# Kernel tuning notes

Measured on AMD Instinct MI355X. Metric: run time of the kernel, lower is better.

Reference implementation:

```python
import math
import jax, jax.numpy as jnp
import numpy as np

B, S, DM = 2, 1024, 1024
H, D = 16, 64
BUCKETS, MAX_POS = 256, 512
SPAN = BUCKETS          # pos_ebd_size = position_buckets
SCALE = math.sqrt(D * 3)  # scale_factor = 1 + len([c2p, p2c])
EPS = 1e-7


def _make_log_bucket_position(rel, bucket_size, max_position):
    # numpy, matches make_log_bucket_position exactly (static, shape-derived)
    sign = np.sign(rel)
    mid = bucket_size // 2
    abs_pos = np.where((rel < mid) & (rel > -mid), mid - 1, np.abs(rel))
    log_pos = np.ceil(np.log(abs_pos / mid) / np.log((max_position - 1) / mid) * (mid - 1)) + mid
    return np.where(abs_pos <= mid, rel, (log_pos * sign)).astype(np.int64)


def _build_relative_position(q_size, k_size):
    rel = np.arange(q_size)[:, None] - np.arange(k_size)[None, :]
    return _make_log_bucket_position(rel, BUCKETS, MAX_POS)  # [q, k]


def setup_inputs() -> dict:
    key = jax.random.key(0)
    ks = jax.random.split(key, 12)
    w = lambda k, sh: (jax.random.normal(k, sh, jnp.float32) * 0.02)
    return {
        "hidden_states": jax.random.normal(ks[0], (B, S, DM), jnp.float32),
        "rel_embeddings": jax.random.normal(ks[1], (2 * SPAN, DM), jnp.float32),
        "Wq": w(ks[2], (DM, DM)), "bq": jnp.zeros((DM,), jnp.float32),
        "Wk": w(ks[3], (DM, DM)), "bk": jnp.zeros((DM,), jnp.float32),
        "Wv": w(ks[4], (DM, DM)), "bv": jnp.zeros((DM,), jnp.float32),
        "Wo": w(ks[5], (DM, DM)), "bo": jnp.zeros((DM,), jnp.float32),
        "ln_w": jnp.ones((DM,), jnp.float32), "ln_b": jnp.zeros((DM,), jnp.float32),
        "attention_mask": jnp.ones((B, 1, S, S), jnp.int32),
    }


def reference(hidden_states, rel_embeddings, Wq, bq, Wk, bk, Wv, bv, Wo, bo, ln_w, ln_b, attention_mask):
    b, s, _ = hidden_states.shape
    heads = lambda x: x.reshape(b, s, H, D).transpose(0, 2, 1, 3)  # [B,H,S,D]
    q = heads(hidden_states @ Wq + bq)
    k = heads(hidden_states @ Wk + bk)
    v = heads(hidden_states @ Wv + bv)

    # content-to-content scores
    scores = jnp.einsum('bhqd,bhkd->bhqk', q, k) / SCALE

    # disentangled relative-position bias (share_att_key=True: reuse key/query proj)
    rel = _build_relative_position(s, s)                      # [S,S] static int
    c2p_idx = np.clip(rel + SPAN, 0, 2 * SPAN - 1)            # [S,S]
    p2c_idx = np.clip(-rel + SPAN, 0, 2 * SPAN - 1)           # [S,S]
    pos_k = (rel_embeddings @ Wk + bk).reshape(2 * SPAN, H, D).transpose(1, 0, 2)  # [H,P,D]
    pos_q = (rel_embeddings @ Wq + bq).reshape(2 * SPAN, H, D).transpose(1, 0, 2)  # [H,P,D]

    qi = np.arange(s)[:, None]  # row index for gather along bucket axis
    c2p = jnp.einsum('bhqd,hpd->bhqp', q, pos_k)              # [B,H,S,2K]
    scores = scores + c2p[:, :, qi, c2p_idx] / SCALE          # gather -> [B,H,S,S]
    p2c = jnp.einsum('bhkd,hpd->bhkp', k, pos_q)              # [B,H,S,2K]
    scores = scores + jnp.swapaxes(p2c[:, :, qi, p2c_idx], -1, -2) / SCALE

    # XSoftmax: masked softmax, masked positions zeroed
    m = attention_mask.astype(bool)
    probs = jax.nn.softmax(jnp.where(m, scores, -jnp.inf), axis=-1)
    probs = jnp.where(m, probs, 0.0)

    ctx = jnp.einsum('bhqk,bhkd->bhqd', probs, v).transpose(0, 2, 1, 3).reshape(b, s, H * D)

    # DebertaV2SelfOutput: dense + (eval-mode dropout = identity) + LayerNorm residual
    h = ctx @ Wo + bo + hidden_states
    mu = h.mean(-1, keepdims=True)
    var = ((h - mu) ** 2).mean(-1, keepdims=True)
    return (h - mu) * jax.lax.rsqrt(var + EPS) * ln_w + ln_b
```

## Files before the change

### kernel.cpp

```cpp
#include <hip/hip_runtime.h>
#include <hip/hip_bf16.h>

#define Sv   1024
#define DMv  1024
#define Hv   16
#define PBv  512
#define INVSCALE 0.07216878364870322f

typedef unsigned short u16;
typedef unsigned int   u32;
typedef short  short8  __attribute__((ext_vector_type(8)));
typedef float  float4v __attribute__((ext_vector_type(4)));

__device__ __forceinline__ float b2f(u16 u) {
    union { u32 u; float f; } c; c.u = ((u32)u) << 16; return c.f;
}
__device__ __forceinline__ u16 f2b(float f) {
    union { float f; u32 u; } c; c.f = f;
    u32 u = c.u;
    return (u16)((u + 0x7fffu + ((u >> 16) & 1u)) >> 16);
}
__device__ __forceinline__ float ldE(const void* p, size_t i, bool f32) {
    return f32 ? ((const float*)p)[i] : b2f(((const u16*)p)[i]);
}

__device__ __forceinline__ void gld16(const u16* g, u16* l) {
    __builtin_amdgcn_global_load_lds(
        (const __attribute__((address_space(1))) void*)g,
        (__attribute__((address_space(3))) void*)l,
        16, 0, 0);
}

__global__ void setup_kernel(const u32* __restrict__ w, int* __restrict__ flag,
                             int* __restrict__ tbl) {
    if (blockIdx.x == 0) {
        int t = threadIdx.x;
        if (t < 64) {
            int c = 0;
            #pragma unroll
            for (int i = 0; i < 4; i++) {
                u32 v = w[t * 4 + i];
                c += (((v >> 23) & 0xFFu) < 0x80u) ? 1 : 0;
            }
            #pragma unroll
            for (int off = 32; off > 0; off >>= 1) c += __shfl_down(c, off, 64);
            if (t == 0) *flag = (c > 128) ? 1 : 0;
        }
        return;
    }
    int i = (blockIdx.x - 1) * 256 + threadIdx.x;
    if (i >= 2047) return;
    int rel = i - 1023;
    const int mid = 128;
    int abs_pos = (rel < mid && rel > -mid) ? (mid - 1) : (rel < 0 ? -rel : rel);
    int bucket;
    if (abs_pos <= mid) {
        bucket = rel;
    } else {
        double lp = ceil(log((double)abs_pos / 128.0) / log(511.0 / 128.0) * 127.0) + 128.0;
        bucket = (int)lp * (rel > 0 ? 1 : -1);
    }
    int idx = bucket + 256;
    idx = idx < 0 ? 0 : (idx > 511 ? 511 : idx);
    tbl[i] = idx;
}

__global__ __launch_bounds__(256) void cvt2_kernel(
    const void* __restrict__ s0, u16* __restrict__ d0,
    const void* __restrict__ s1, u16* __restrict__ d1,
    const int* __restrict__ flagp)
{
    bool f32 = (*flagp != 0);
    const void* src; u16* dst; size_t i;
    if (blockIdx.x < 1024) {
        src = s0; dst = d0;
        i = ((size_t)blockIdx.x * 256 + threadIdx.x) * 8;
    } else {
        src = s1; dst = d1;
        i = ((size_t)(blockIdx.x - 1024) * 256 + threadIdx.x) * 8;
    }
    if (f32) {
        const float* s = (const float*)src + i;
        float4 a = *(const float4*)s;
        float4 b = *(const float4*)(s + 4);
        uint4 o = make_uint4(f2b(a.x) | (f2b(a.y) << 16), f2b(a.z) | (f2b(a.w) << 16),
                             f2b(b.x) | (f2b(b.y) << 16), f2b(b.z) | (f2b(b.w) << 16));
        *(uint4*)(dst + i) = o;
    } else {
        *(uint4*)(dst + i) = *(const uint4*)((const u16*)src + i);
    }
}

__global__ __launch_bounds__(256) void transpose_cvt(
    const void* __restrict__ S0, const void* __restrict__ S1,
    const void* __restrict__ S2, const void* __restrict__ S3,
    u16* __restrict__ out, u16* __restrict__ out3,
    const int* __restrict__ flagp)
{
    bool f32 = (*flagp != 0);
    int z = blockIdx.z;
    const void* S = (z == 0) ? S0 : (z == 1) ? S1 : (z == 2) ? S2 : S3;
    u16* O = (z < 3) ? (out + (size_t)z * 1048576) : out3;
    int k0 = blockIdx.x * 64, n0 = blockIdx.y * 64;
    __shared__ u16 Ls[64][72];
    int t = threadIdx.x;
    int r = t >> 2, cseg = (t & 3) * 16;

    u16 v[16];
    size_t base = (size_t)(k0 + r) * 1024 + n0 + cseg;
    if (f32) {
        const float* p = (const float*)S + base;
        #pragma unroll
        for (int i = 0; i < 16; i += 4) {
            float4 f = *(const float4*)(p + i);
            v[i] = f2b(f.x); v[i + 1] = f2b(f.y); v[i + 2] = f2b(f.z); v[i + 3] = f2b(f.w);
        }
    } else {
        const u16* p = (const u16*)S + base;
        uint4 a = *(const uint4*)p, b = *(const uint4*)(p + 8);
        u32 wd[8] = {a.x, a.y, a.z, a.w, b.x, b.y, b.z, b.w};
        #pragma unroll
        for (int i = 0; i < 8; i++) { v[2 * i] = (u16)(wd[i] & 0xffff); v[2 * i + 1] = (u16)(wd[i] >> 16); }
    }
    #pragma unroll
    for (int i = 0; i < 16; i++) Ls[cseg + i][r] = v[i];
    __syncthreads();

    int n = t >> 2, kseg = (t & 3) * 16;
    u16* op = O + (size_t)(n0 + n) * 1024 + k0 + kseg;
    *(uint4*)op       = *(const uint4*)&Ls[n][kseg];
    *(uint4*)(op + 8) = *(const uint4*)&Ls[n][kseg + 8];
}

__global__ __launch_bounds__(256) void wgemm_bt(
    const u16* __restrict__ A,
    const u16* __restrict__ B0, const u16* __restrict__ B1, const u16* __restrict__ B2,
    const void* __restrict__ b0, const void* __restrict__ b1, const void* __restrict__ b2,
    u16* __restrict__ O0, u16* __restrict__ O1, u16* __restrict__ O2,
    const int* __restrict__ flagp, int vseg, int sseg)
{
    bool f32 = (*flagp != 0);
    __shared__ u16 As[128][64];
    __shared__ u16 Bs[128][64];

    int t = threadIdx.x;
    int seg = blockIdx.x >> 3;
    int n0  = (blockIdx.x & 7) * 128;
    int m0  = blockIdx.y * 128;
    const u16* Bt = (seg == 0) ? B0 : (seg == 1) ? B1 : B2;
    const void* bi = (seg == 0) ? b0 : (seg == 1) ? b1 : b2;
    u16* O = (seg == 0) ? O0 : (seg == 1) ? O1 : O2;
    float es = (seg == sseg) ? INVSCALE : 1.0f;

    int w = t >> 6, lane = t & 63;
    int quad = lane >> 4, l16 = lane & 15;
    int wm = (w >> 1) * 64, wn = (w & 1) * 64;

    float4v acc[4][4];
    #pragma unroll
    for (int i = 0; i < 4; i++)
        #pragma unroll
        for (int j = 0; j < 4; j++)
            acc[i][j] = (float4v){0.f, 0.f, 0.f, 0.f};

    int lr8  = lane >> 3;
    int lcol = (lane & 7) * 8;
    const u16* ap0 = A  + (size_t)(m0 + w * 32 + lr8) * 1024 + lcol;
    const u16* bp0 = Bt + (size_t)(n0 + w * 32 + lr8) * 1024 + lcol;

    for (int k0 = 0; k0 < 1024; k0 += 64) {
        __syncthreads();
        #pragma unroll
        for (int i = 0; i < 4; i++) {
            gld16(ap0 + (size_t)(i * 8) * 1024 + k0, &As[w * 32 + i * 8][0]);
            gld16(bp0 + (size_t)(i * 8) * 1024 + k0, &Bs[w * 32 + i * 8][0]);
        }
        __syncthreads();

        #pragma unroll
        for (int kk = 0; kk < 64; kk += 32) {
            short8 af[4], bf[4];
            #pragma unroll
            for (int i = 0; i < 4; i++)
                af[i] = *(const short8*)&As[wm + i * 16 + l16][kk + quad * 8];
            #pragma unroll
            for (int j = 0; j < 4; j++)
                bf[j] = *(const short8*)&Bs[wn + j * 16 + l16][kk + quad * 8];
            #pragma unroll
            for (int j = 0; j < 4; j++)
                #pragma unroll
                for (int i = 0; i < 4; i++)
                    acc[i][j] = __builtin_amdgcn_mfma_f32_16x16x32_bf16(af[i], bf[j], acc[i][j], 0, 0, 0);
        }
    }

    if (seg == vseg) {
        #pragma unroll
        for (int j = 0; j < 4; j++) {
            int ncol = n0 + wn + j * 16 + l16;
            float bv = ldE(bi, ncol, f32);
            u16* obase = O + (size_t)(ncol >> 6) * 131072 + (size_t)(ncol & 63) * 2048;
            #pragma unroll
            for (int i = 0; i < 4; i++) {
                int rbase = m0 + wm + i * 16 + quad * 4;
                u32 w0 = (u32)f2b((acc[i][j][0] + bv) * es) | ((u32)f2b((acc[i][j][1] + bv) * es) << 16);
                u32 w1 = (u32)f2b((acc[i][j][2] + bv) * es) | ((u32)f2b((acc[i][j][3] + bv) * es) << 16);
                *(uint2*)(obase + rbase) = make_uint2(w0, w1);
            }
        }
    } else {
        #pragma unroll
        for (int j = 0; j < 4; j++) {
            int ncol = n0 + wn + j * 16 + l16;
            float bv = ldE(bi, ncol, f32);
            #pragma unroll
            for (int i = 0; i < 4; i++) {
                int rbase = m0 + wm + i * 16 + quad * 4;
                #pragma unroll
                for (int r = 0; r < 4; r++)
                    O[(size_t)(rbase + r) * 1024 + ncol] = f2b((acc[i][j][r] + bv) * es);
            }
        }
    }
}

__global__ __launch_bounds__(256) void wgemm_bt_m64(
    const u16* __restrict__ A, const u16* __restrict__ Bt,
    const void* __restrict__ bi, u16* __restrict__ O,
    const int* __restrict__ flagp)
{
    bool f32 = (*flagp != 0);
    __shared__ u16 As[64][64];
    __shared__ u16 Bs[128][64];

    int t = threadIdx.x;
    int n0 = blockIdx.x * 128;
    int m0 = blockIdx.y * 64;

    int w = t >> 6, lane = t & 63;
    int quad = lane >> 4, l16 = lane & 15;
    int wm = (w >> 1) * 32, wn = (w & 1) * 64;

    float4v acc[2][4];
    #pragma unroll
    for (int i = 0; i < 2; i++)
        #pragma unroll
        for (int j = 0; j < 4; j++)
            acc[i][j] = (float4v){0.f, 0.f, 0.f, 0.f};

    int lr8  = lane >> 3;
    int lcol = (lane & 7) * 8;
    const u16* ap0 = A  + (size_t)(m0 + w * 16 + lr8) * 1024 + lcol;
    const u16* bp0 = Bt + (size_t)(n0 + w * 32 + lr8) * 1024 + lcol;

    for (int k0 = 0; k0 < 1024; k0 += 64) {
        __syncthreads();
        #pragma unroll
        for (int i = 0; i < 2; i++)
            gld16(ap0 + (size_t)(i * 8) * 1024 + k0, &As[w * 16 + i * 8][0]);
        #pragma unroll
        for (int i = 0; i < 4; i++)
            gld16(bp0 + (size_t)(i * 8) * 1024 + k0, &Bs[w * 32 + i * 8][0]);
        __syncthreads();

        #pragma unroll
        for (int kk = 0; kk < 64; kk += 32) {
            short8 af[2], bf[4];
            #pragma unroll
            for (int i = 0; i < 2; i++)
                af[i] = *(const short8*)&As[wm + i * 16 + l16][kk + quad * 8];
            #pragma unroll
            for (int j = 0; j < 4; j++)
                bf[j] = *(const short8*)&Bs[wn + j * 16 + l16][kk + quad * 8];
            #pragma unroll
            for (int j = 0; j < 4; j++)
                #pragma unroll
                for (int i = 0; i < 2; i++)
                    acc[i][j] = __builtin_amdgcn_mfma_f32_16x16x32_bf16(af[i], bf[j], acc[i][j], 0, 0, 0);
        }
    }

    #pragma unroll
    for (int j = 0; j < 4; j++) {
        int ncol = n0 + wn + j * 16 + l16;
        float bv = ldE(bi, ncol, f32);
        #pragma unroll
        for (int i = 0; i < 2; i++) {
            int rbase = m0 + wm + i * 16 + quad * 4;
            #pragma unroll
            for (int r = 0; r < 4; r++)
                O[(size_t)(rbase + r) * 1024 + ncol] = f2b(acc[i][j][r] + bv);
        }
    }
}

__global__ __launch_bounds__(256) void pos_score_mfma(
    const u16* __restrict__ Xq, const u16* __restrict__ Xk,
    const u16* __restrict__ PK, const u16* __restrict__ PQ,
    u16* __restrict__ outq, u16* __restrict__ outk,
    size_t xStride, size_t oStride)
{
    int zT = blockIdx.z & 1, b = blockIdx.z >> 1;
    int h  = blockIdx.x >> 2;
    int a  = blockIdx.x & 3;
    int m0 = zT ? a * 128 : blockIdx.y * 128;
    int n0 = zT ? blockIdx.y * 128 : a * 128;
    const u16* Am = zT ? PQ : (Xq + (size_t)b * xStride);
    const u16* Bn = zT ? (Xk + (size_t)b * xStride) : PK;
    u16* out      = (zT ? outk : outq) + (size_t)b * oStride;
    size_t cs     = zT ? (size_t)Sv : (size_t)PBv;

    __shared__ u16 As[128][64];
    __shared__ u16 Bs[128][64];
    int t = threadIdx.x;

    int w = t >> 6, lane = t & 63;
    int quad = lane >> 4, l16 = lane & 15;
    int wm = (w >> 1) * 64, wn = (w & 1) * 64;

    int lr8  = lane >> 3;
    int lcol = (lane & 7) * 8;
    {
        const u16* xp = Am + (size_t)(m0 + w * 32 + lr8) * 1024 + h * 64 + lcol;
        const u16* pp = Bn + (size_t)(n0 + w * 32 + lr8) * 1024 + h * 64 + lcol;
        #pragma unroll
        for (int i = 0; i < 4; i++) {
            gld16(xp + (size_t)(i * 8) * 1024, &As[w * 32 + i * 8][0]);
            gld16(pp + (size_t)(i * 8) * 1024, &Bs[w * 32 + i * 8][0]);
        }
    }
    __syncthreads();

    float4v acc[4][4];
    #pragma unroll
    for (int i = 0; i < 4; i++)
        #pragma unroll
        for (int j = 0; j < 4; j++)
            acc[i][j] = (float4v){0.f, 0.f, 0.f, 0.f};

    #pragma unroll
    for (int k0 = 0; k0 < 64; k0 += 32) {
        short8 af[4], bf[4];
        #pragma unroll
        for (int i = 0; i < 4; i++)
            af[i] = *(const short8*)&As[wm + i * 16 + l16][k0 + quad * 8];
        #pragma unroll
        for (int j = 0; j < 4; j++)
            bf[j] = *(const short8*)&Bs[wn + j * 16 + l16][k0 + quad * 8];
        #pragma unroll
        for (int j = 0; j < 4; j++)
            #pragma unroll
            for (int i = 0; i < 4; i++)
                acc[i][j] = __builtin_amdgcn_mfma_f32_16x16x32_bf16(af[i], bf[j], acc[i][j], 0, 0, 0);
    }

    u16* oh = out + (size_t)h * ((size_t)PBv * Sv);
    #pragma unroll
    for (int j = 0; j < 4; j++) {
        int jc = n0 + wn + j * 16 + l16;
        #pragma unroll
        for (int i = 0; i < 4; i++) {
            int rbase = m0 + wm + i * 16 + quad * 4;
            #pragma unroll
            for (int r = 0; r < 4; r++)
                oh[(size_t)(rbase + r) * cs + jc] = f2b(acc[i][j][r]);
        }
    }
}

__global__ __launch_bounds__(256, 2) void attn6_kernel(
    const u16* __restrict__ Qg, const u16* __restrict__ Kg,
    const u16* __restrict__ Vtg,
    const u16* __restrict__ C2Pg,
    const u16* __restrict__ P2Ctg,
    const int* __restrict__ tbl, u16* __restrict__ CTXg,
    size_t biasStride)
{
    int bz = blockIdx.z;
    const u16* Q    = Qg    + (size_t)bz * Sv * DMv;
    const u16* K    = Kg    + (size_t)bz * Sv * DMv;
    const u16* Vt   = Vtg   + (size_t)bz * 1024;
    const u16* C2P  = C2Pg  + (size_t)bz * biasStride;
    const u16* P2Ct = P2Ctg + (size_t)bz * biasStride;
    u16* CTX        = CTXg  + (size_t)bz * Sv * DMv;

    __shared__ u16 Kc[2][64][64];
    __shared__ u16 Vc[2][64][64];
    __shared__ u16 Qc[32][72];
    __shared__ u16 Pb[4][16][72];
    __shared__ short stbl[2047];
    __shared__ float msh[2][2][16], lsh[2][2][16];

    int t = threadIdx.x, w = t >> 6, lane = t & 63;
    int qg = w >> 1, ks = w & 1;
    int quad = lane >> 4, l16 = lane & 15;
    int h = blockIdx.y, q0 = blockIdx.x * 32;

    for (int i = t; i < 2047; i += 256) stbl[i] = (short)tbl[i];
    {
        int row = t >> 3, dseg = (t & 7) * 8;
        *(uint4*)&Qc[row][dseg] =
            *(const uint4*)(Q + (size_t)(q0 + row) * DMv + h * 64 + dseg);
    }
    __syncthreads();

    short8 afq0 = *(const short8*)&Qc[qg * 16 + l16][quad * 8];
    short8 afq1 = *(const short8*)&Qc[qg * 16 + l16][quad * 8 + 32];

    int qrow = q0 + qg * 16 + quad * 4;
    const u16* c2p_h  = C2P  + (size_t)h * (Sv * PBv);
    const u16* p2ct_h = P2Ct + (size_t)h * (PBv * Sv);
    const u16* vt_h   = Vt   + (size_t)h * 131072;

    int sspw = w & 1, rbase = (w >> 1) * 32;
    int lrow = lane >> 3;
    int lsw  = ((lane & 7) ^ lrow) * 8;
    int s0   = (quad ^ (l16 & 7)) * 8;

    float m[4] = {-1e30f, -1e30f, -1e30f, -1e30f};
    float l[4] = {0.f, 0.f, 0.f, 0.f};
    float4v Ov[4];
    #pragma unroll
    for (int j = 0; j < 4; j++) Ov[j] = (float4v){0.f, 0.f, 0.f, 0.f};

    {
        const u16* kb = K + (size_t)(sspw * 512) * 1024 + h * 64;
        #pragma unroll
        for (int i = 0; i < 4; i++) {
            int r = rbase + i * 8;
            gld16(kb + (size_t)(r + lrow) * 1024 + lsw, &Kc[sspw][r][0]);
        }
    }
    u32 cpre[4][4], ppre[4][4];
    #pragma unroll
    for (int j = 0; j < 4; j++) {
        int k = ks * 512 + j * 16 + l16;
        #pragma unroll
        for (int r = 0; r < 4; r++) {
            int q = qrow + r;
            int idx = stbl[q - k + 1023];
            cpre[j][r] = c2p_h[(size_t)q * PBv + idx];
            ppre[j][r] = p2ct_h[(size_t)idx * Sv + k];
        }
    }

    for (int c = 0; c < 8; c++) {
        __syncthreads();

        {
            const u16* vb = vt_h + sspw * 512 + c * 64;
            #pragma unroll
            for (int i = 0; i < 4; i++) {
                int r = rbase + i * 8;
                gld16(vb + (size_t)(r + lrow) * 2048 + lsw, &Vc[sspw][r][0]);
            }
        }

        int kb = ks * 512 + c * 64;
        float p[4][4];
        #pragma unroll
        for (int j = 0; j < 4; j++) {
            short8 bk0 = *(const short8*)&Kc[ks][j * 16 + l16][s0];
            short8 bk1 = *(const short8*)&Kc[ks][j * 16 + l16][s0 ^ 32];
            float4v a = (float4v){0.f, 0.f, 0.f, 0.f};
            a = __builtin_amdgcn_mfma_f32_16x16x32_bf16(afq0, bk0, a, 0, 0, 0);
            a = __builtin_amdgcn_mfma_f32_16x16x32_bf16(afq1, bk1, a, 0, 0, 0);
            #pragma unroll
            for (int r = 0; r < 4; r++) p[j][r] = a[r];
        }
        #pragma unroll
        for (int j = 0; j < 4; j++)
            #pragma unroll
            for (int r = 0; r < 4; r++)
                p[j][r] = p[j][r] + b2f((u16)cpre[j][r]) + b2f((u16)ppre[j][r]);
        if (c < 7) {
            #pragma unroll
            for (int j = 0; j < 4; j++) {
                int k2 = ks * 512 + (c + 1) * 64 + j * 16 + l16;
                #pragma unroll
                for (int r = 0; r < 4; r++) {
                    int q = qrow + r;
                    int idx = stbl[q - k2 + 1023];
                    cpre[j][r] = c2p_h[(size_t)q * PBv + idx];
                    ppre[j][r] = p2ct_h[(size_t)idx * Sv + k2];
                }
            }
        }

        float corr[4];
        #pragma unroll
        for (int r = 0; r < 4; r++) {
            float v = fmaxf(fmaxf(p[0][r], p[1][r]), fmaxf(p[2][r], p[3][r]));
            v = fmaxf(v, __shfl_xor(v, 1, 64));
            v = fmaxf(v, __shfl_xor(v, 2, 64));
            v = fmaxf(v, __shfl_xor(v, 4, 64));
            v = fmaxf(v, __shfl_xor(v, 8, 64));
            float nm = fmaxf(m[r], v);
            corr[r] = __expf(m[r] - nm);
            m[r] = nm;
        }
        #pragma unroll
        for (int r = 0; r < 4; r++) {
            #pragma unroll
            for (int j = 0; j < 4; j++) p[j][r] = __expf(p[j][r] - m[r]);
            float s = p[0][r] + p[1][r] + p[2][r] + p[3][r];
            s += __shfl_xor(s, 1, 64);
            s += __shfl_xor(s, 2, 64);
            s += __shfl_xor(s, 4, 64);
            s += __shfl_xor(s, 8, 64);
            l[r] = l[r] * corr[r] + s;
            #pragma unroll
            for (int j = 0; j < 4; j++) Ov[j][r] *= corr[r];
        }
        #pragma unroll
        for (int j = 0; j < 4; j++)
            #pragma unroll
            for (int r = 0; r < 4; r++)
                Pb[w][quad * 4 + r][j * 16 + l16] = f2b(p[j][r]);

        __syncthreads();

        if (c < 7) {
            const u16* kb2 = K + (size_t)(sspw * 512 + (c + 1) * 64) * 1024 + h * 64;
            #pragma unroll
            for (int i = 0; i < 4; i++) {
                int r = rbase + i * 8;
                gld16(kb2 + (size_t)(r + lrow) * 1024 + lsw, &Kc[sspw][r][0]);
            }
        }

        short8 ap0 = *(const short8*)&Pb[w][l16][quad * 8];
        short8 ap1 = *(const short8*)&Pb[w][l16][quad * 8 + 32];
        #pragma unroll
        for (int j = 0; j < 4; j++) {
            short8 bv0 = *(const short8*)&Vc[ks][j * 16 + l16][s0];
            short8 bv1 = *(const short8*)&Vc[ks][j * 16 + l16][s0 ^ 32];
            Ov[j] = __builtin_amdgcn_mfma_f32_16x16x32_bf16(ap0, bv0, Ov[j], 0, 0, 0);
            Ov[j] = __builtin_amdgcn_mfma_f32_16x16x32_bf16(ap1, bv1, Ov[j], 0, 0, 0);
        }
    }

    if (l16 == 0) {
        #pragma unroll
        for (int r = 0; r < 4; r++) {
            msh[qg][ks][quad * 4 + r] = m[r];
            lsh[qg][ks][quad * 4 + r] = l[r];
        }
    }
    __syncthreads();
    float scl[4];
    #pragma unroll
    for (int r = 0; r < 4; r++) {
        int row = quad * 4 + r;
        float m0 = msh[qg][0][row], m1 = msh[qg][1][row];
        float M = fmaxf(m0, m1);
        float L = lsh[qg][0][row] * __expf(m0 - M) + lsh[qg][1][row] * __expf(m1 - M);
        scl[r] = __expf(m[r] - M) / L;
    }
    float* Obuf = (float*)&Kc[0][0][0];
    if (ks == 1) {
        #pragma unroll
        for (int j = 0; j < 4; j++)
            #pragma unroll
            for (int r = 0; r < 4; r++)
                Obuf[(qg * 16 + quad * 4 + r) * 66 + j * 16 + l16] = Ov[j][r] * scl[r];
    }
    __syncthreads();
    if (ks == 0) {
        #pragma unroll
        for (int j = 0; j < 4; j++)
            #pragma unroll
            for (int r = 0; r < 4; r++) {
                float v = Ov[j][r] * scl[r]
                        + Obuf[(qg * 16 + quad * 4 + r) * 66 + j * 16 + l16];
                CTX[(size_t)(qrow + r) * DMv + h * 64 + j * 16 + l16] = f2b(v);
            }
    }
}

__global__ __launch_bounds__(256) void ln_kernel(
    const u16* __restrict__ Hb, const void* __restrict__ hidden,
    const void* __restrict__ lnw, const void* __restrict__ lnb,
    void* __restrict__ out, const int* __restrict__ flagp)
{
    bool f32 = (*flagp != 0);
    int row = blockIdx.x;
    int t = threadIdx.x;
    const u16* hp = Hb + (size_t)row * DMv;

    uint2 hv = *(const uint2*)(hp + t * 4);
    float x[4];
    x[0] = b2f(hv.x & 0xffff); x[1] = b2f(hv.x >> 16);
    x[2] = b2f(hv.y & 0xffff); x[3] = b2f(hv.y >> 16);
    size_t rb = (size_t)row * DMv + t * 4;
    if (f32) {
        float4 xv = *(const float4*)((const float*)hidden + rb);
        x[0] += xv.x; x[1] += xv.y; x[2] += xv.z; x[3] += xv.w;
    } else {
        uint2 xv = *(const uint2*)((const u16*)hidden + rb);
        x[0] += b2f(xv.x & 0xffff); x[1] += b2f(xv.x >> 16);
        x[2] += b2f(xv.y & 0xffff); x[3] += b2f(xv.y >> 16);
    }

    float s1 = x[0] + x[1] + x[2] + x[3];
    float s2 = x[0] * x[0] + x[1] * x[1] + x[2] * x[2] + x[3] * x[3];
    #pragma unroll
    for (int off = 32; off > 0; off >>= 1) {
        s1 += __shfl_down(s1, off, 64);
        s2 += __shfl_down(s2, off, 64);
    }
    __shared__ float r1[4], r2[4];
    int wave = t >> 6, lane = t & 63;
    if (lane == 0) { r1[wave] = s1; r2[wave] = s2; }
    __syncthreads();
    float ts1 = r1[0] + r1[1] + r1[2] + r1[3];
    float ts2 = r2[0] + r2[1] + r2[2] + r2[3];
    float mu  = ts1 * (1.0f / DMv);
    float var = fmaxf(ts2 * (1.0f / DMv) - mu * mu, 0.f);
    float rs  = rsqrtf(var + 1e-7f);
    #pragma unroll
    for (int i = 0; i < 4; i++) {
        int c = t * 4 + i;
        float v = (x[i] - mu) * rs * ldE(lnw, c, f32) + ldE(lnb, c, f32);
        if (f32) ((float*)out)[(size_t)row * DMv + c] = v;
        else     ((u16*)out)[(size_t)row * DMv + c] = f2b(v);
    }
}

extern "C" void kernel_launch(void* const* d_in, const int* in_sizes, int n_in,
                              void* d_out, int out_size, void* d_ws, size_t ws_size,
                              hipStream_t stream) {
    const void* hidden = d_in[0];
    const void* rel    = d_in[1];
    const void* Wq = d_in[2];  const void* bq = d_in[3];
    const void* Wk = d_in[4];  const void* bk = d_in[5];
    const void* Wv = d_in[6];  const void* bv = d_in[7];
    const void* Wo = d_in[8];  const void* bo = d_in[9];
    const void* lnw = d_in[10]; const void* lnb = d_in[11];

    const size_t MB = 1u << 20;
    char* ws = (char*)d_ws;
    int* FLAG = (int*)ws;
    int* TBL  = (int*)(ws + 1024);
    char* base = ws + (64 << 10);
    u16* Qb   = (u16*)(base + 0 * MB);
    u16* Kb   = (u16*)(base + 4 * MB);
    u16* Vt   = (u16*)(base + 8 * MB);
    u16* CTX  = (u16*)(base + 12 * MB);
    u16* Xb   = (u16*)(base + 12 * MB);
    u16* PKb  = (u16*)(base + 16 * MB);
    u16* PQb  = (u16*)(base + 17 * MB);
    u16* HB   = (u16*)(base + 16 * MB);
    u16* C2P  = (u16*)(base + 18 * MB);
    u16* P2Ct = (u16*)(base + 34 * MB);
    u16* WqT  = (u16*)(base + 34 * MB);
    u16* WkT  = (u16*)(base + 36 * MB);
    u16* WvT  = (u16*)(base + 38 * MB);
    u16* relb = (u16*)(base + 40 * MB);
    u16* WoT  = (u16*)(base + 50 * MB);
    const size_t BSTRIDE = ((size_t)34 * MB) / 2;
    bool big = ws_size >= ((size_t)85 << 20);

    dim3 blk(256);

    setup_kernel<<<9, blk, 0, stream>>>((const u32*)Wq, FLAG, TBL);
    cvt2_kernel<<<1280, blk, 0, stream>>>(hidden, Xb, rel, relb, FLAG);
    transpose_cvt<<<dim3(16, 16, 4), blk, 0, stream>>>(
        Wq, Wk, Wv, Wo, WqT, WoT, FLAG);

    wgemm_bt<<<dim3(24, 16), blk, 0, stream>>>(
        Xb, WqT, WkT, WvT, bq, bk, bv, Qb, Kb, Vt, FLAG, 2, 0);
    wgemm_bt<<<dim3(16, 4), blk, 0, stream>>>(
        relb, WkT, WqT, nullptr, bk, bq, nullptr, PKb, PQb, nullptr, FLAG, -1, 1);

    if (big) {
        pos_score_mfma<<<dim3(64, 8, 4), blk, 0, stream>>>(
            Qb, Kb, PKb, PQb, C2P, P2Ct, (size_t)Sv * DMv, BSTRIDE);
        attn6_kernel<<<dim3(32, 16, 2), blk, 0, stream>>>(
            Qb, Kb, Vt, C2P, P2Ct, TBL, CTX, BSTRIDE);
    } else {
        for (int b = 0; b < 2; b++) {
            size_t off = (size_t)b * Sv * DMv;
            pos_score_mfma<<<dim3(64, 8, 2), blk, 0, stream>>>(
                Qb + off, Kb + off, PKb, PQb, C2P, P2Ct, 0, 0);
            attn6_kernel<<<dim3(32, 16, 1), blk, 0, stream>>>(
                Qb + off, Kb + off, Vt + (size_t)b * 1024, C2P, P2Ct, TBL,
                CTX + off, 0);
        }
    }

    wgemm_bt_m64<<<dim3(8, 32), blk, 0, stream>>>(CTX, WoT, bo, HB, FLAG);
    ln_kernel<<<2048, blk, 0, stream>>>(HB, hidden, lnw, lnb, d_out, FLAG);
}
```

Baseline: 266.7 us.

## Precompute dense combined positional bias in a fused expand kernel

```diff
diff --git a/kernel.cpp b/kernel.cpp
--- a/kernel.cpp
+++ b/kernel.cpp
@@ -294,76 +294,133 @@
     }
 }
 
-__global__ __launch_bounds__(256) void pos_score_mfma(
-    const u16* __restrict__ Xq, const u16* __restrict__ Xk,
+__global__ __launch_bounds__(256, 2) void bias_expand(
+    const u16* __restrict__ Qg, const u16* __restrict__ Kg,
     const u16* __restrict__ PK, const u16* __restrict__ PQ,
-    u16* __restrict__ outq, u16* __restrict__ outk,
-    size_t xStride, size_t oStride)
+    const int* __restrict__ tbl, u16* __restrict__ SB)
 {
-    int zT = blockIdx.z & 1, b = blockIdx.z >> 1;
-    int h  = blockIdx.x >> 2;
-    int a  = blockIdx.x & 3;
-    int m0 = zT ? a * 128 : blockIdx.y * 128;
-    int n0 = zT ? blockIdx.y * 128 : a * 128;
-    const u16* Am = zT ? PQ : (Xq + (size_t)b * xStride);
-    const u16* Bn = zT ? (Xk + (size_t)b * xStride) : PK;
-    u16* out      = (zT ? outk : outq) + (size_t)b * oStride;
-    size_t cs     = zT ? (size_t)Sv : (size_t)PBv;
-
-    __shared__ u16 As[128][64];
-    __shared__ u16 Bs[128][64];
-    int t = threadIdx.x;
-
-    int w = t >> 6, lane = t & 63;
+    __shared__ u16 Qs[32][64];
+    __shared__ u16 PKw[96][64];
+    __shared__ u16 PQw[96][64];
+    __shared__ u16 Kch[64][64];
+    __shared__ u16 C2Po[32][96];
+    __shared__ u16 P2Co[96][64];
+    __shared__ short stbl[2047];
+
+    int t = threadIdx.x, w = t >> 6, lane = t & 63;
     int quad = lane >> 4, l16 = lane & 15;
-    int wm = (w >> 1) * 64, wn = (w & 1) * 64;
-
-    int lr8  = lane >> 3;
-    int lcol = (lane & 7) * 8;
-    {
-        const u16* xp = Am + (size_t)(m0 + w * 32 + lr8) * 1024 + h * 64 + lcol;
-        const u16* pp = Bn + (size_t)(n0 + w * 32 + lr8) * 1024 + h * 64 + lcol;
-        #pragma unroll
-        for (int i = 0; i < 4; i++) {
-            gld16(xp + (size_t)(i * 8) * 1024, &As[w * 32 + i * 8][0]);
-            gld16(pp + (size_t)(i * 8) * 1024, &Bs[w * 32 + i * 8][0]);
-        }
-    }
+    int q0 = blockIdx.x * 32, h = blockIdx.y, b = blockIdx.z;
+    const u16* Q = Qg + (size_t)b * Sv * DMv;
+    const u16* K = Kg + (size_t)b * Sv * DMv;
+    u16* sb = SB + (((size_t)b * Hv + h) * Sv + q0) * Sv;
+
+    for (int i = t; i < 2047; i += 256) stbl[i] = (short)tbl[i];
+
+    int lrow = lane >> 3, lcol = (lane & 7) * 8;
+    gld16(Q + (size_t)(q0 + w * 8 + lrow) * 1024 + h * 64 + lcol, &Qs[w * 8][0]);
     __syncthreads();
 
-    float4v acc[4][4];
-    #pragma unroll
-    for (int i = 0; i < 4; i++)
-        #pragma unroll
-        for (int j = 0; j < 4; j++)
-            acc[i][j] = (float4v){0.f, 0.f, 0.f, 0.f};
-
-    #pragma unroll
-    for (int k0 = 0; k0 < 64; k0 += 32) {
-        short8 af[4], bf[4];
-        #pragma unroll
-        for (int i = 0; i < 4; i++)
-            af[i] = *(const short8*)&As[wm + i * 16 + l16][k0 + quad * 8];
-        #pragma unroll
-        for (int j = 0; j < 4; j++)
-            bf[j] = *(const short8*)&Bs[wn + j * 16 + l16][k0 + quad * 8];
-        #pragma unroll
-        for (int j = 0; j < 4; j++)
-            #pragma unroll
-            for (int i = 0; i < 4; i++)
-                acc[i][j] = __builtin_amdgcn_mfma_f32_16x16x32_bf16(af[i], bf[j], acc[i][j], 0, 0, 0);
-    }
-
-    u16* oh = out + (size_t)h * ((size_t)PBv * Sv);
-    #pragma unroll
-    for (int j = 0; j < 4; j++) {
-        int jc = n0 + wn + j * 16 + l16;
-        #pragma unroll
-        for (int i = 0; i < 4; i++) {
-            int rbase = m0 + wm + i * 16 + quad * 4;
-            #pragma unroll
-            for (int r = 0; r < 4; r++)
-                oh[(size_t)(rbase + r) * cs + jc] = f2b(acc[i][j][r]);
+    short8 aq0[2], aq1[2];
+    if (w < 2) {
+        #pragma unroll
+        for (int i = 0; i < 2; i++) {
+            aq0[i] = *(const short8*)&Qs[i * 16 + l16][quad * 8];
+            aq1[i] = *(const short8*)&Qs[i * 16 + l16][quad * 8 + 32];
+        }
+    }
+
+    int eq = t >> 3;
+    int ekk = (t & 7) * 8;
+
+    for (int c = 0; c < 16; c++) {
+        int kc = c * 64;
+        int jmin = q0 - kc - 63 + 1023;
+        int idxlo = stbl[jmin];
+        if (idxlo > 416) idxlo = 416;
+
+        __syncthreads();
+
+        #pragma unroll
+        for (int i = 0; i < 3; i++) {
+            int r = w * 24 + i * 8;
+            gld16(PK + (size_t)(idxlo + r + lrow) * 1024 + h * 64 + lcol, &PKw[r][0]);
+            gld16(PQ + (size_t)(idxlo + r + lrow) * 1024 + h * 64 + lcol, &PQw[r][0]);
+        }
+        #pragma unroll
+        for (int i = 0; i < 2; i++) {
+            int r = w * 16 + i * 8;
+            gld16(K + (size_t)(kc + r + lrow) * 1024 + h * 64 + lcol, &Kch[r][0]);
+        }
+        __syncthreads();
+
+        if (w < 2) {
+            float4v acc[2][3];
+            #pragma unroll
+            for (int i = 0; i < 2; i++)
+                #pragma unroll
+                for (int j = 0; j < 3; j++)
+                    acc[i][j] = (float4v){0.f, 0.f, 0.f, 0.f};
+            #pragma unroll
+            for (int j = 0; j < 3; j++) {
+                int nf = w * 3 + j;
+                short8 bf0 = *(const short8*)&PKw[nf * 16 + l16][quad * 8];
+                short8 bf1 = *(const short8*)&PKw[nf * 16 + l16][quad * 8 + 32];
+                #pragma unroll
+                for (int i = 0; i < 2; i++) {
+                    acc[i][j] = __builtin_amdgcn_mfma_f32_16x16x32_bf16(aq0[i], bf0, acc[i][j], 0, 0, 0);
+                    acc[i][j] = __builtin_amdgcn_mfma_f32_16x16x32_bf16(aq1[i], bf1, acc[i][j], 0, 0, 0);
+                }
+            }
+            #pragma unroll
+            for (int j = 0; j < 3; j++)
+                #pragma unroll
+                for (int i = 0; i < 2; i++)
+                    #pragma unroll
+                    for (int r = 0; r < 4; r++)
+                        C2Po[i * 16 + quad * 4 + r][(w * 3 + j) * 16 + l16] = f2b(acc[i][j][r]);
+        } else {
+            float4v acc[3][4];
+            #pragma unroll
+            for (int i = 0; i < 3; i++)
+                #pragma unroll
+                for (int j = 0; j < 4; j++)
+                    acc[i][j] = (float4v){0.f, 0.f, 0.f, 0.f};
+            #pragma unroll
+            for (int i = 0; i < 3; i++) {
+                int mf = (w - 2) * 3 + i;
+                short8 af0 = *(const short8*)&PQw[mf * 16 + l16][quad * 8];
+                short8 af1 = *(const short8*)&PQw[mf * 16 + l16][quad * 8 + 32];
+                #pragma unroll
+                for (int j = 0; j < 4; j++) {
+                    short8 bf0 = *(const short8*)&Kch[j * 16 + l16][quad * 8];
+                    short8 bf1 = *(const short8*)&Kch[j * 16 + l16][quad * 8 + 32];
+                    acc[i][j] = __builtin_amdgcn_mfma_f32_16x16x32_bf16(af0, bf0, acc[i][j], 0, 0, 0);
+                    acc[i][j] = __builtin_amdgcn_mfma_f32_16x16x32_bf16(af1, bf1, acc[i][j], 0, 0, 0);
+                }
+            }
+            #pragma unroll
+            for (int i = 0; i < 3; i++)
+                #pragma unroll
+                for (int j = 0; j < 4; j++)
+                    #pragma unroll
+                    for (int r = 0; r < 4; r++)
+                        P2Co[((w - 2) * 3 + i) * 16 + quad * 4 + r][j * 16 + l16] = f2b(acc[i][j][r]);
+        }
+        __syncthreads();
+
+        {
+            int jbase = (q0 + eq) - (kc + ekk) + 1023;
+            u32 res[4];
+            #pragma unroll
+            for (int i = 0; i < 8; i += 2) {
+                int d0 = stbl[jbase - i] - idxlo;
+                int d1 = stbl[jbase - i - 1] - idxlo;
+                float v0 = b2f(C2Po[eq][d0]) + b2f(P2Co[d0][ekk + i]);
+                float v1 = b2f(C2Po[eq][d1]) + b2f(P2Co[d1][ekk + i + 1]);
+                res[i >> 1] = (u32)f2b(v0) | ((u32)f2b(v1) << 16);
+            }
+            *(uint4*)(sb + (size_t)eq * Sv + kc + ekk) =
+                make_uint4(res[0], res[1], res[2], res[3]);
         }
     }
 }
@@ -371,24 +428,19 @@
 __global__ __launch_bounds__(256, 2) void attn6_kernel(
     const u16* __restrict__ Qg, const u16* __restrict__ Kg,
     const u16* __restrict__ Vtg,
-    const u16* __restrict__ C2Pg,
-    const u16* __restrict__ P2Ctg,
-    const int* __restrict__ tbl, u16* __restrict__ CTXg,
-    size_t biasStride)
+    const u16* __restrict__ SB,
+    u16* __restrict__ CTXg)
 {
     int bz = blockIdx.z;
     const u16* Q    = Qg    + (size_t)bz * Sv * DMv;
     const u16* K    = Kg    + (size_t)bz * Sv * DMv;
     const u16* Vt   = Vtg   + (size_t)bz * 1024;
-    const u16* C2P  = C2Pg  + (size_t)bz * biasStride;
-    const u16* P2Ct = P2Ctg + (size_t)bz * biasStride;
     u16* CTX        = CTXg  + (size_t)bz * Sv * DMv;
 
     __shared__ u16 Kc[2][64][64];
     __shared__ u16 Vc[2][64][64];
     __shared__ u16 Qc[32][72];
     __shared__ u16 Pb[4][16][72];
-    __shared__ short stbl[2047];
     __shared__ float msh[2][2][16], lsh[2][2][16];
 
     int t = threadIdx.x, w = t >> 6, lane = t & 63;
@@ -396,7 +448,6 @@
     int quad = lane >> 4, l16 = lane & 15;
     int h = blockIdx.y, q0 = blockIdx.x * 32;
 
-    for (int i = t; i < 2047; i += 256) stbl[i] = (short)tbl[i];
     {
         int row = t >> 3, dseg = (t & 7) * 8;
         *(uint4*)&Qc[row][dseg] =
@@ -408,9 +459,8 @@
     short8 afq1 = *(const short8*)&Qc[qg * 16 + l16][quad * 8 + 32];
 
     int qrow = q0 + qg * 16 + quad * 4;
-    const u16* c2p_h  = C2P  + (size_t)h * (Sv * PBv);
-    const u16* p2ct_h = P2Ct + (size_t)h * (PBv * Sv);
-    const u16* vt_h   = Vt   + (size_t)h * 131072;
+    const u16* sb_h = SB + ((size_t)(bz * Hv + h) * Sv) * Sv;
+    const u16* vt_h = Vt + (size_t)h * 131072;
 
     int sspw = w & 1, rbase = (w >> 1) * 32;
     int lrow = lane >> 3;
@@ -431,17 +481,13 @@
             gld16(kb + (size_t)(r + lrow) * 1024 + lsw, &Kc[sspw][r][0]);
         }
     }
-    u32 cpre[4][4], ppre[4][4];
+    u32 spre[4][4];
     #pragma unroll
     for (int j = 0; j < 4; j++) {
         int k = ks * 512 + j * 16 + l16;
         #pragma unroll
-        for (int r = 0; r < 4; r++) {
-            int q = qrow + r;
-            int idx = stbl[q - k + 1023];
-            cpre[j][r] = c2p_h[(size_t)q * PBv + idx];
-            ppre[j][r] = p2ct_h[(size_t)idx * Sv + k];
-        }
+        for (int r = 0; r < 4; r++)
+            spre[j][r] = sb_h[(size_t)(qrow + r) * Sv + k];
     }
 
     for (int c = 0; c < 8; c++) {
@@ -456,7 +502,6 @@
             }
         }
 
-        int kb = ks * 512 + c * 64;
         float p[4][4];
         #pragma unroll
         for (int j = 0; j < 4; j++) {
@@ -472,18 +517,14 @@
         for (int j = 0; j < 4; j++)
             #pragma unroll
             for (int r = 0; r < 4; r++)
-                p[j][r] = p[j][r] + b2f((u16)cpre[j][r]) + b2f((u16)ppre[j][r]);
+                p[j][r] = p[j][r] + b2f((u16)spre[j][r]);
         if (c < 7) {
             #pragma unroll
             for (int j = 0; j < 4; j++) {
                 int k2 = ks * 512 + (c + 1) * 64 + j * 16 + l16;
                 #pragma unroll
-                for (int r = 0; r < 4; r++) {
-                    int q = qrow + r;
-                    int idx = stbl[q - k2 + 1023];
-                    cpre[j][r] = c2p_h[(size_t)q * PBv + idx];
-                    ppre[j][r] = p2ct_h[(size_t)idx * Sv + k2];
-                }
+                for (int r = 0; r < 4; r++)
+                    spre[j][r] = sb_h[(size_t)(qrow + r) * Sv + k2];
             }
         }
 
@@ -651,15 +692,12 @@
     u16* PKb  = (u16*)(base + 16 * MB);
     u16* PQb  = (u16*)(base + 17 * MB);
     u16* HB   = (u16*)(base + 16 * MB);
-    u16* C2P  = (u16*)(base + 18 * MB);
-    u16* P2Ct = (u16*)(base + 34 * MB);
     u16* WqT  = (u16*)(base + 34 * MB);
     u16* WkT  = (u16*)(base + 36 * MB);
     u16* WvT  = (u16*)(base + 38 * MB);
     u16* relb = (u16*)(base + 40 * MB);
     u16* WoT  = (u16*)(base + 50 * MB);
-    const size_t BSTRIDE = ((size_t)34 * MB) / 2;
-    bool big = ws_size >= ((size_t)85 << 20);
+    u16* SB   = (u16*)(base + 52 * MB);
 
     dim3 blk(256);
 
@@ -673,21 +711,11 @@
     wgemm_bt<<<dim3(16, 4), blk, 0, stream>>>(
         relb, WkT, WqT, nullptr, bk, bq, nullptr, PKb, PQb, nullptr, FLAG, -1, 1);
 
-    if (big) {
-        pos_score_mfma<<<dim3(64, 8, 4), blk, 0, stream>>>(
-            Qb, Kb, PKb, PQb, C2P, P2Ct, (size_t)Sv * DMv, BSTRIDE);
-        attn6_kernel<<<dim3(32, 16, 2), blk, 0, stream>>>(
-            Qb, Kb, Vt, C2P, P2Ct, TBL, CTX, BSTRIDE);
-    } else {
-        for (int b = 0; b < 2; b++) {
-            size_t off = (size_t)b * Sv * DMv;
-            pos_score_mfma<<<dim3(64, 8, 2), blk, 0, stream>>>(
-                Qb + off, Kb + off, PKb, PQb, C2P, P2Ct, 0, 0);
-            attn6_kernel<<<dim3(32, 16, 1), blk, 0, stream>>>(
-                Qb + off, Kb + off, Vt + (size_t)b * 1024, C2P, P2Ct, TBL,
-                CTX + off, 0);
-        }
-    }
+    bias_expand<<<dim3(32, 16, 2), blk, 0, stream>>>(
+        Qb, Kb, PKb, PQb, TBL, SB);
+
+    attn6_kernel<<<dim3(32, 16, 2), blk, 0, stream>>>(
+        Qb, Kb, Vt, SB, CTX);
 
     wgemm_bt_m64<<<dim3(8, 32), blk, 0, stream>>>(CTX, WoT, bo, HB, FLAG);
     ln_kernel<<<2048, blk, 0, stream>>>(HB, hidden, lnw, lnb, d_out, FLAG);
```

Result: slower. 298.4 us (+11.9%).
